# Performance work log

Measured on AMD Instinct MI355X. Metric: run time of the kernel, lower is better.

Reference implementation:

```python
import jax, jax.numpy as jnp
import numpy as np

V, E, H, B, S = 32000, 512, 1024, 128, 512
NEG = -1e9


def setup_inputs() -> dict:
    key = jax.random.key(0)
    ks = jax.random.split(key, 12)
    s = 0.02
    return {
        "previous_word": jax.random.randint(ks[0], (B, 1), 0, V),
        "h_0": jax.random.normal(ks[1], (B, H), jnp.float32),
        "c_0": jax.random.normal(ks[2], (B, H), jnp.float32),
        "ctx": jax.random.normal(ks[3], (B, S, H), jnp.float32),
        "ctx_mask": jnp.zeros((B, S), dtype=bool),
        "emb": jax.random.normal(ks[4], (V, E), jnp.float32) * s,
        "W_ih": jax.random.normal(ks[5], (4 * H, E), jnp.float32) * s,
        "W_hh": jax.random.normal(ks[6], (4 * H, H), jnp.float32) * s,
        "b_ih": jnp.zeros((4 * H,), jnp.float32),
        "b_hh": jnp.zeros((4 * H,), jnp.float32),
        "W_in": jax.random.normal(ks[7], (H, H), jnp.float32) * s,
        "W_out": jax.random.normal(ks[8], (H, 2 * H), jnp.float32) * s,
        "W_dec": jax.random.normal(ks[9], (V, H), jnp.float32) * s,
        "b_dec": jnp.zeros((V,), jnp.float32),
    }


def reference(previous_word, h_0, c_0, ctx, ctx_mask, emb, W_ih, W_hh, b_ih, b_hh, W_in, W_out, W_dec, b_dec):
    # embedding lookup + squeeze; dropout is identity in eval mode
    x = emb[previous_word[:, 0]]                       # [B, E]
    # LSTMCell: gate order i, f, g, o (PyTorch convention)
    gates = x @ W_ih.T + b_ih + h_0 @ W_hh.T + b_hh    # [B, 4H]
    i, f, g, o = jnp.split(gates, 4, axis=1)
    i = jax.nn.sigmoid(i)
    f = jax.nn.sigmoid(f)
    g = jnp.tanh(g)
    o = jax.nn.sigmoid(o)
    c_1 = f * c_0 + i * g
    h_1 = o * jnp.tanh(c_1)
    # SoftDotAttention
    target = h_1 @ W_in.T                               # [B, H]
    attn = jnp.einsum('bsh,bh->bs', ctx, target)        # [B, S]
    attn = jnp.where(ctx_mask, NEG, attn)
    alpha = jax.nn.softmax(attn, axis=1)
    weighted = jnp.einsum('bs,bsh->bh', alpha, ctx)     # [B, H]
    h_tilde = jnp.tanh(jnp.concatenate([weighted, h_1], axis=1) @ W_out.T)
    logit = h_tilde @ W_dec.T + b_dec                   # [B, V]
    return (h_1, c_1, alpha, logit)
```

## Files before the change

### kernel.cpp

```cpp
#include <hip/hip_runtime.h>
#include <hip/hip_bf16.h>
#include <cstdint>

#define NEG_BIG (-1.0e9f)

typedef __attribute__((ext_vector_type(8))) short short8_t;
typedef __attribute__((ext_vector_type(4))) float f32x4;

typedef __attribute__((address_space(1))) const unsigned int gu32_t;
typedef __attribute__((address_space(3))) unsigned int lu32_t;

__device__ __forceinline__ short f2bf(float x) {
  union { float f; unsigned u; } v; v.f = x;
  unsigned r = v.u + 0x7fffu + ((v.u >> 16) & 1u);
  return (short)(r >> 16);
}
__device__ __forceinline__ float sigmoidf_(float x) { return 1.0f / (1.0f + __expf(-x)); }

__device__ __forceinline__ void lds_barrier() {
  asm volatile("s_waitcnt lgkmcnt(0)\n\ts_barrier" ::: "memory");
}
__device__ __forceinline__ void block_barrier() {
  asm volatile("" ::: "memory");
  __builtin_amdgcn_s_barrier();
  asm volatile("" ::: "memory");
}

__global__ void k_pack_a1(const int* __restrict__ prev, const float* __restrict__ emb,
                          const float* __restrict__ h0, short* __restrict__ A1) {
  int t = blockIdx.x * 256 + threadIdx.x;
  if (t >= 128 * 1536) return;
  int b = t / 1536, k = t - b * 1536;
  float v = (k < 512) ? emb[(size_t)prev[b] * 512 + k] : h0[b * 1024 + (k - 512)];
  A1[t] = f2bf(v);
}

template <int MB, int WN, int EPI>
__launch_bounds__(256, 2)
__global__ void k_gemm(const short* __restrict__ A, int lda,
                       const float* __restrict__ Wa, int ldwa, int Ka,
                       const float* __restrict__ Wb, int ldwb, int Ktot,
                       const float* __restrict__ bias0, const float* __restrict__ bias1,
                       float* __restrict__ outF, short* __restrict__ outB, int ldo,
                       int kstride, size_t pstride) {
  constexpr int BN = WN * 16;
  constexpr int MREP = (MB == 128) ? 2 * WN : 1;
  constexpr int AU = MB / 32;
  constexpr int WLOADS = (BN * 64) / 1024;
  __shared__ __align__(16) short lA[2][MB * 64];
  __shared__ __align__(16) short lW[2][BN * 64];
  const int kc = blockIdx.z;
  A += (size_t)kc * kstride;
  Wa += (size_t)kc * kstride;
  if (outF) outF += (size_t)kc * pstride;
  const int tid = threadIdx.x;
  const int wid = tid >> 6, l = tid & 63, l15 = l & 15, khalf = l >> 4;
  const int nblk = blockIdx.x;
  const int mrow0 = blockIdx.y * MB;
  const int m_wave = (WN == 1) ? wid * (MB / 4) : 0;
  const int nb_local = (WN == 4) ? wid * 16 : 0;

  const int arow = (MB == 128) ? (tid >> 1) : (tid >> 2);
  const int apart = (MB == 128) ? (tid & 1) : (tid & 3);
  const int abase = apart * (AU * 16);
  const int aswz = (arow & 7) << 4;
  const short* Arow = A + (size_t)(mrow0 + arow) * lda + apart * (AU * 8);

  int wn_[WLOADS], wkq_[WLOADS];
#pragma unroll
  for (int j = 0; j < WLOADS; ++j) {
    int idx = j * 1024 + tid * 4;
    wn_[j] = idx >> 6;
    wkq_[j] = idx & 63;
  }

  f32x4 acc[MREP];
#pragma unroll
  for (int r = 0; r < MREP; ++r) acc[r] = (f32x4){0.f, 0.f, 0.f, 0.f};

  short8_t aR[AU];
  float4 wR[WLOADS];

  auto stage_regs = [&](int k0) {
#pragma unroll
    for (int q = 0; q < AU; ++q) aR[q] = *(const short8_t*)(Arow + k0 + q * 8);
#pragma unroll
    for (int j = 0; j < WLOADS; ++j) {
      int kg = k0 + wkq_[j];
      const float* p = (kg < Ka) ? (Wa + (size_t)(nblk * BN + wn_[j]) * ldwa + kg)
                                 : (Wb + (size_t)(nblk * BN + wn_[j]) * ldwb + (kg - Ka));
      wR[j] = *(const float4*)p;
    }
  };
  auto write_lds = [&](int buf) {
    char* drow = (char*)lA[buf] + arow * 128;
#pragma unroll
    for (int q = 0; q < AU; ++q)
      *(short8_t*)(drow + ((abase + q * 16) ^ aswz)) = aR[q];
#pragma unroll
    for (int j = 0; j < WLOADS; ++j) {
      short4 h4;
      h4.x = f2bf(wR[j].x); h4.y = f2bf(wR[j].y); h4.z = f2bf(wR[j].z); h4.w = f2bf(wR[j].w);
      *(short4*)((char*)lW[buf] + wn_[j] * 128 + ((wkq_[j] * 2) ^ ((wn_[j] & 7) << 4))) = h4;
    }
  };
  auto compute = [&](int buf) {
#pragma unroll
    for (int ks = 0; ks < 2; ++ks) {
      const int ubyte = ks * 64 + khalf * 16;
      const int nrow = nb_local + l15;
      short8_t bfrag = *(const short8_t*)((char*)lW[buf] + nrow * 128 + (ubyte ^ ((nrow & 7) << 4)));
#pragma unroll
      for (int r = 0; r < MREP; ++r) {
        const int mrow = m_wave + r * 16 + l15;
        short8_t afrag = *(const short8_t*)((char*)lA[buf] + mrow * 128 + (ubyte ^ ((mrow & 7) << 4)));
        acc[r] = __builtin_amdgcn_mfma_f32_16x16x32_bf16(afrag, bfrag, acc[r], 0, 0, 0);
      }
    }
  };

  const int NT = Ktot >> 6;
  stage_regs(0);
  write_lds(0);
  for (int t = 0; t < NT; ++t) {
    const int cur = t & 1;
    if (t + 1 < NT) stage_regs((t + 1) << 6);
    lds_barrier();
    compute(cur);
    if (t + 1 < NT) write_lds(cur ^ 1);
  }

  const int n = nblk * BN + nb_local + l15;
  float bias = 0.f;
  if (bias0) bias = bias0[n];
  if (bias1) bias += bias1[n];
#pragma unroll
  for (int r = 0; r < MREP; ++r) {
    int mb = mrow0 + m_wave + r * 16 + khalf * 4;
#pragma unroll
    for (int e = 0; e < 4; ++e) {
      float v = acc[r][e] + bias;
      if (EPI == 1) {
        outB[(size_t)(mb + e) * ldo + n] = f2bf(tanhf(v));
      } else {
        outF[(size_t)(mb + e) * ldo + n] = v;
      }
    }
  }
}

__global__ void k_lstm(const float* __restrict__ gates, const float* __restrict__ c0,
                       float* __restrict__ h1_out, float* __restrict__ c1_out,
                       short* __restrict__ A3) {
  int t = blockIdx.x * 256 + threadIdx.x;
  int b = t >> 10, h = t & 1023;
  const float* g = gates + (size_t)b * 4096;
  float ig = sigmoidf_(g[h]);
  float fg = sigmoidf_(g[1024 + h]);
  float gg = tanhf(g[2048 + h]);
  float og = sigmoidf_(g[3072 + h]);
  float c1 = fg * c0[t] + ig * gg;
  float h1 = og * tanhf(c1);
  c1_out[t] = c1;
  h1_out[t] = h1;
  A3[(size_t)b * 2048 + 1024 + h] = f2bf(h1);
}

__launch_bounds__(256, 2)
__global__ void k_attn(const float* __restrict__ ctx, const float* __restrict__ tp,
                       const unsigned char* __restrict__ mask,
                       float* __restrict__ scores, float* __restrict__ part) {
  __shared__ __align__(16) float lds[2][8 * 1024];
  const int b = blockIdx.x >> 2, chunk = blockIdx.x & 3;
  const int tid = threadIdx.x;
  const int wid = tid >> 6, l = tid & 63;
  float4 t4[4], w4[4];
#pragma unroll
  for (int j = 0; j < 4; ++j) {
    float4 a = {0.f, 0.f, 0.f, 0.f};
#pragma unroll
    for (int p = 0; p < 4; ++p) {
      const float4 v = *(const float4*)(tp + (size_t)p * 131072 + (size_t)b * 1024 + j * 256 + l * 4);
      a.x += v.x; a.y += v.y; a.z += v.z; a.w += v.w;
    }
    t4[j] = a;
    w4[j].x = 0.f; w4[j].y = 0.f; w4[j].z = 0.f; w4[j].w = 0.f;
  }
  float m = -INFINITY, lsum = 0.f;
  const int s0 = chunk * 128;
  const float* cb = ctx + ((size_t)b * 512 + s0) * 1024;
  const unsigned char* mk = mask + (size_t)b * 512 + s0;

  auto stage = [&](int buf, int tt) {
    const char* src = (const char*)(cb + (size_t)tt * 8192);
    char* dst = (char*)&lds[buf][0];
#pragma unroll
    for (int i = 0; i < 8; ++i) {
      const int off = i * 4096 + tid * 16;
      __builtin_amdgcn_global_load_lds((gu32_t*)(src + off), (lu32_t*)(dst + off), 16, 0, 0);
    }
  };

  stage(0, 0);
  int buf = 0;
  for (int t = 0; t < 16; ++t) {
    if (t < 15) {
      stage(buf ^ 1, t + 1);
      asm volatile("s_waitcnt vmcnt(8)" ::: "memory");
    } else {
      asm volatile("s_waitcnt vmcnt(0)" ::: "memory");
    }
    block_barrier();
#pragma unroll
    for (int rr = 0; rr < 2; ++rr) {
      const int r = wid * 2 + rr;
      const float* row = &lds[buf][r * 1024];
      float4 c0 = *(const float4*)(row + l * 4);
      float4 c1 = *(const float4*)(row + 256 + l * 4);
      float4 c2 = *(const float4*)(row + 512 + l * 4);
      float4 c3 = *(const float4*)(row + 768 + l * 4);
      float p = c0.x * t4[0].x + c0.y * t4[0].y + c0.z * t4[0].z + c0.w * t4[0].w +
                c1.x * t4[1].x + c1.y * t4[1].y + c1.z * t4[1].z + c1.w * t4[1].w +
                c2.x * t4[2].x + c2.y * t4[2].y + c2.z * t4[2].z + c2.w * t4[2].w +
                c3.x * t4[3].x + c3.y * t4[3].y + c3.z * t4[3].z + c3.w * t4[3].w;
#pragma unroll
      for (int off = 32; off > 0; off >>= 1) p += __shfl_xor(p, off);
      const int sg = t * 8 + r;
      if (mk[sg]) p = NEG_BIG;
      if (l == 0) scores[(size_t)b * 512 + s0 + sg] = p;
      float mn = fmaxf(m, p);
      float scale = __expf(m - mn);
      float e = __expf(p - mn);
      lsum = lsum * scale + e;
      w4[0].x = w4[0].x * scale + e * c0.x; w4[0].y = w4[0].y * scale + e * c0.y;
      w4[0].z = w4[0].z * scale + e * c0.z; w4[0].w = w4[0].w * scale + e * c0.w;
      w4[1].x = w4[1].x * scale + e * c1.x; w4[1].y = w4[1].y * scale + e * c1.y;
      w4[1].z = w4[1].z * scale + e * c1.z; w4[1].w = w4[1].w * scale + e * c1.w;
      w4[2].x = w4[2].x * scale + e * c2.x; w4[2].y = w4[2].y * scale + e * c2.y;
      w4[2].z = w4[2].z * scale + e * c2.z; w4[2].w = w4[2].w * scale + e * c2.w;
      w4[3].x = w4[3].x * scale + e * c3.x; w4[3].y = w4[3].y * scale + e * c3.y;
      w4[3].z = w4[3].z * scale + e * c3.z; w4[3].w = w4[3].w * scale + e * c3.w;
      m = mn;
    }
    block_barrier();
    buf ^= 1;
  }
  float* pp = part + ((size_t)b * 16 + (chunk * 4 + wid)) * 1028;
#pragma unroll
  for (int j = 0; j < 4; ++j) *(float4*)(pp + j * 256 + l * 4) = w4[j];
  if (l == 0) { pp[1024] = m; pp[1025] = lsum; }
}

__launch_bounds__(256, 4)
__global__ void k_finish(const float* __restrict__ scores, const float* __restrict__ part,
                         float* __restrict__ alpha, short* __restrict__ A3) {
  __shared__ float sm[16], sl[16];
  int b = blockIdx.x, t = threadIdx.x;
  if (t < 16) {
    sm[t] = part[((size_t)b * 16 + t) * 1028 + 1024];
    sl[t] = part[((size_t)b * 16 + t) * 1028 + 1025];
  }
  __syncthreads();
  float M = -INFINITY;
#pragma unroll
  for (int i = 0; i < 16; ++i) M = fmaxf(M, sm[i]);
  float scl[16];
  float L = 0.f;
#pragma unroll
  for (int i = 0; i < 16; ++i) {
    scl[i] = __expf(sm[i] - M);
    L += sl[i] * scl[i];
  }
  float inv = 1.0f / L;
  float s0 = scores[(size_t)b * 512 + t];
  float s1 = scores[(size_t)b * 512 + 256 + t];
  alpha[(size_t)b * 512 + t] = __expf(s0 - M) * inv;
  alpha[(size_t)b * 512 + 256 + t] = __expf(s1 - M) * inv;
  float ax = 0.f, ay = 0.f, az = 0.f, aw = 0.f;
#pragma unroll
  for (int i = 0; i < 16; ++i) {
    const float4 w = *(const float4*)(part + ((size_t)b * 16 + i) * 1028 + t * 4);
    ax += scl[i] * w.x; ay += scl[i] * w.y; az += scl[i] * w.z; aw += scl[i] * w.w;
  }
  short4 o4;
  o4.x = f2bf(ax * inv); o4.y = f2bf(ay * inv); o4.z = f2bf(az * inv); o4.w = f2bf(aw * inv);
  *(short4*)(A3 + (size_t)b * 2048 + t * 4) = o4;
}

__global__ void k_htilde(const float* __restrict__ wp, short* __restrict__ ht) {
  int t = blockIdx.x * 256 + threadIdx.x;
  float s = 0.f;
#pragma unroll
  for (int p = 0; p < 8; ++p) s += wp[(size_t)p * 131072 + t];
  ht[t] = f2bf(tanhf(s));
}

extern "C" void kernel_launch(void* const* d_in, const int* in_sizes, int n_in,
                              void* d_out, int out_size, void* d_ws, size_t ws_size,
                              hipStream_t stream) {
  const int* prev = (const int*)d_in[0];
  const float* h0 = (const float*)d_in[1];
  const float* c0 = (const float*)d_in[2];
  const float* ctx = (const float*)d_in[3];
  const unsigned char* mask = (const unsigned char*)d_in[4];
  const float* emb = (const float*)d_in[5];
  const float* W_ih = (const float*)d_in[6];
  const float* W_hh = (const float*)d_in[7];
  const float* b_ih = (const float*)d_in[8];
  const float* b_hh = (const float*)d_in[9];
  const float* W_in = (const float*)d_in[10];
  const float* W_out = (const float*)d_in[11];
  const float* W_dec = (const float*)d_in[12];
  const float* b_dec = (const float*)d_in[13];

  float* out_h1 = (float*)d_out;
  float* out_c1 = out_h1 + 128 * 1024;
  float* out_alpha = out_c1 + 128 * 1024;
  float* out_logit = out_alpha + 128 * 512;

  char* ws = (char*)d_ws;
  short* A3 = (short*)(ws + 0x000000);
  float* scores = (float*)(ws + 0x100000);
  float* tp = (float*)(ws + 0x200000);
  float* part = (float*)(ws + 0x400000);
  float* wp = (float*)(ws + 0xD00000);
  float* gates = (float*)(ws + 0x1100000);
  short* A1 = (short*)(ws + 0x1300000);
  short* htilde = (short*)(ws + 0x1400000);

  k_pack_a1<<<768, 256, 0, stream>>>(prev, emb, h0, A1);
  k_gemm<128, 1, 0><<<dim3(256, 1, 1), 256, 0, stream>>>(
      A1, 1536, W_ih, 512, 512, W_hh, 1024, 1536, b_ih, b_hh, gates, nullptr, 4096, 0, 0);
  k_lstm<<<512, 256, 0, stream>>>(gates, c0, out_h1, out_c1, A3);
  k_gemm<128, 1, 0><<<dim3(64, 1, 4), 256, 0, stream>>>(
      A3 + 1024, 2048, W_in, 1024, 1 << 30, W_in, 1024, 256, nullptr, nullptr, tp, nullptr,
      1024, 256, (size_t)131072);
  k_attn<<<512, 256, 0, stream>>>(ctx, tp, mask, scores, part);
  k_finish<<<128, 256, 0, stream>>>(scores, part, out_alpha, A3);
  k_gemm<128, 1, 0><<<dim3(64, 1, 8), 256, 0, stream>>>(
      A3, 2048, W_out, 2048, 1 << 30, W_out, 2048, 256, nullptr, nullptr, wp, nullptr,
      1024, 256, (size_t)131072);
  k_htilde<<<512, 256, 0, stream>>>(wp, htilde);
  k_gemm<128, 4, 0><<<dim3(500, 1, 1), 256, 0, stream>>>(
      htilde, 1024, W_dec, 1024, 1024, W_dec, 1024, 1024, b_dec, nullptr, out_logit, nullptr,
      32000, 0, 0);
}
```

Baseline: 134.3 us.

## Fuse embedding gather into gate GEMM and pre-reduce attention partials per block

Replaces the separate pack kernel plus generic gate GEMM with a dedicated kernel that gathers embedding rows and h_0 directly from global memory, converts them to bf16 in registers and stages them in LDS, removing one launch and the A1 round trip. Inside the attention kernel the four per-wave online-softmax partials are merged through LDS before being written, so the finish kernel reads 4 partials per batch instead of 16. This cuts partial-buffer traffic, at the cost of an extra block-wide barrier and LDS pass at the end of attention. The fused GEMM also redoes the bf16 conversion of the A tile in every one of its 256 blocks.

```diff
diff --git a/kernel.cpp b/kernel.cpp
--- a/kernel.cpp
+++ b/kernel.cpp
@@ -26,13 +26,89 @@
   asm volatile("" ::: "memory");
 }
 
-__global__ void k_pack_a1(const int* __restrict__ prev, const float* __restrict__ emb,
-                          const float* __restrict__ h0, short* __restrict__ A1) {
-  int t = blockIdx.x * 256 + threadIdx.x;
-  if (t >= 128 * 1536) return;
-  int b = t / 1536, k = t - b * 1536;
-  float v = (k < 512) ? emb[(size_t)prev[b] * 512 + k] : h0[b * 1024 + (k - 512)];
-  A1[t] = f2bf(v);
+__launch_bounds__(256, 2)
+__global__ void k_ggemm(const int* __restrict__ prev, const float* __restrict__ emb,
+                        const float* __restrict__ h0,
+                        const float* __restrict__ W_ih, const float* __restrict__ W_hh,
+                        const float* __restrict__ b_ih, const float* __restrict__ b_hh,
+                        float* __restrict__ gates) {
+  __shared__ __align__(16) short lA[2][128 * 64];
+  __shared__ __align__(16) short lW[2][16 * 64];
+  const int tid = threadIdx.x;
+  const int wid = tid >> 6, l = tid & 63, l15 = l & 15, khalf = l >> 4;
+  const int nblk = blockIdx.x;
+
+  const int arow = tid >> 1, apart = tid & 1;
+  const int aswz = (arow & 7) << 4;
+  const float* embrow = emb + (size_t)prev[arow] * 512;
+  const float* h0row = h0 + (size_t)arow * 1024;
+
+  const int wn = (tid * 4) >> 6;
+  const int wkq = (tid * 4) & 63;
+  const float* wih = W_ih + (size_t)(nblk * 16 + wn) * 512;
+  const float* whh = W_hh + (size_t)(nblk * 16 + wn) * 1024;
+
+  f32x4 acc[2];
+  acc[0] = (f32x4){0.f, 0.f, 0.f, 0.f};
+  acc[1] = (f32x4){0.f, 0.f, 0.f, 0.f};
+
+  float4 aF[8], wR;
+  auto stage_regs = [&](int k0) {
+    const int col0 = k0 + apart * 32;
+    const float* asrc = (col0 < 512) ? (embrow + col0) : (h0row + (col0 - 512));
+#pragma unroll
+    for (int q = 0; q < 8; ++q) aF[q] = *(const float4*)(asrc + q * 4);
+    const int kg = k0 + wkq;
+    wR = (kg < 512) ? *(const float4*)(wih + kg) : *(const float4*)(whh + (kg - 512));
+  };
+  auto write_lds = [&](int buf) {
+    char* drow = (char*)lA[buf] + arow * 128;
+#pragma unroll
+    for (int q = 0; q < 4; ++q) {
+      short8_t s;
+      s[0] = f2bf(aF[2 * q].x); s[1] = f2bf(aF[2 * q].y);
+      s[2] = f2bf(aF[2 * q].z); s[3] = f2bf(aF[2 * q].w);
+      s[4] = f2bf(aF[2 * q + 1].x); s[5] = f2bf(aF[2 * q + 1].y);
+      s[6] = f2bf(aF[2 * q + 1].z); s[7] = f2bf(aF[2 * q + 1].w);
+      *(short8_t*)(drow + ((apart * 64 + q * 16) ^ aswz)) = s;
+    }
+    short4 h4;
+    h4.x = f2bf(wR.x); h4.y = f2bf(wR.y); h4.z = f2bf(wR.z); h4.w = f2bf(wR.w);
+    *(short4*)((char*)lW[buf] + wn * 128 + ((wkq * 2) ^ ((wn & 7) << 4))) = h4;
+  };
+  auto compute = [&](int buf) {
+#pragma unroll
+    for (int ks = 0; ks < 2; ++ks) {
+      const int ubyte = ks * 64 + khalf * 16;
+      short8_t bfrag = *(const short8_t*)((char*)lW[buf] + l15 * 128 + (ubyte ^ ((l15 & 7) << 4)));
+#pragma unroll
+      for (int r = 0; r < 2; ++r) {
+        const int mrow = wid * 32 + r * 16 + l15;
+        short8_t afrag = *(const short8_t*)((char*)lA[buf] + mrow * 128 + (ubyte ^ ((mrow & 7) << 4)));
+        acc[r] = __builtin_amdgcn_mfma_f32_16x16x32_bf16(afrag, bfrag, acc[r], 0, 0, 0);
+      }
+    }
+  };
+
+  stage_regs(0);
+  write_lds(0);
+  for (int t = 0; t < 24; ++t) {
+    const int cur = t & 1;
+    if (t + 1 < 24) stage_regs((t + 1) << 6);
+    lds_barrier();
+    compute(cur);
+    if (t + 1 < 24) write_lds(cur ^ 1);
+  }
+
+  const int n = nblk * 16 + l15;
+  const float bias = b_ih[n] + b_hh[n];
+#pragma unroll
+  for (int r = 0; r < 2; ++r) {
+    int mb = wid * 32 + r * 16 + khalf * 4;
+#pragma unroll
+    for (int e = 0; e < 4; ++e)
+      gates[(size_t)(mb + e) * 4096 + n] = acc[r][e] + bias;
+  }
 }
 
 template <int MB, int WN, int EPI>
@@ -171,6 +247,7 @@
                        const unsigned char* __restrict__ mask,
                        float* __restrict__ scores, float* __restrict__ part) {
   __shared__ __align__(16) float lds[2][8 * 1024];
+  __shared__ float sml[8];
   const int b = blockIdx.x >> 2, chunk = blockIdx.x & 3;
   const int tid = threadIdx.x;
   const int wid = tid >> 6, l = tid & 63;
@@ -245,29 +322,45 @@
     block_barrier();
     buf ^= 1;
   }
-  float* pp = part + ((size_t)b * 16 + (chunk * 4 + wid)) * 1028;
-#pragma unroll
-  for (int j = 0; j < 4; ++j) *(float4*)(pp + j * 256 + l * 4) = w4[j];
-  if (l == 0) { pp[1024] = m; pp[1025] = lsum; }
+
+  float* cbuf = &lds[0][0];
+#pragma unroll
+  for (int j = 0; j < 4; ++j) *(float4*)(cbuf + wid * 1024 + j * 256 + l * 4) = w4[j];
+  if (l == 0) { sml[wid] = m; sml[4 + wid] = lsum; }
+  __syncthreads();
+  const float M = fmaxf(fmaxf(sml[0], sml[1]), fmaxf(sml[2], sml[3]));
+  const float sc0 = __expf(sml[0] - M), sc1 = __expf(sml[1] - M);
+  const float sc2 = __expf(sml[2] - M), sc3 = __expf(sml[3] - M);
+  const float L = sml[4] * sc0 + sml[5] * sc1 + sml[6] * sc2 + sml[7] * sc3;
+  const float4 v0 = *(const float4*)(cbuf + 0 * 1024 + tid * 4);
+  const float4 v1 = *(const float4*)(cbuf + 1 * 1024 + tid * 4);
+  const float4 v2 = *(const float4*)(cbuf + 2 * 1024 + tid * 4);
+  const float4 v3 = *(const float4*)(cbuf + 3 * 1024 + tid * 4);
+  float4 o;
+  o.x = v0.x * sc0 + v1.x * sc1 + v2.x * sc2 + v3.x * sc3;
+  o.y = v0.y * sc0 + v1.y * sc1 + v2.y * sc2 + v3.y * sc3;
+  o.z = v0.z * sc0 + v1.z * sc1 + v2.z * sc2 + v3.z * sc3;
+  o.w = v0.w * sc0 + v1.w * sc1 + v2.w * sc2 + v3.w * sc3;
+  float* pp = part + ((size_t)b * 4 + chunk) * 1028;
+  *(float4*)(pp + tid * 4) = o;
+  if (tid == 0) { pp[1024] = M; pp[1025] = L; }
 }
 
 __launch_bounds__(256, 4)
 __global__ void k_finish(const float* __restrict__ scores, const float* __restrict__ part,
                          float* __restrict__ alpha, short* __restrict__ A3) {
-  __shared__ float sm[16], sl[16];
+  __shared__ float sm[4], sl[4];
   int b = blockIdx.x, t = threadIdx.x;
-  if (t < 16) {
-    sm[t] = part[((size_t)b * 16 + t) * 1028 + 1024];
-    sl[t] = part[((size_t)b * 16 + t) * 1028 + 1025];
+  if (t < 4) {
+    sm[t] = part[((size_t)b * 4 + t) * 1028 + 1024];
+    sl[t] = part[((size_t)b * 4 + t) * 1028 + 1025];
   }
   __syncthreads();
-  float M = -INFINITY;
-#pragma unroll
-  for (int i = 0; i < 16; ++i) M = fmaxf(M, sm[i]);
-  float scl[16];
+  float M = fmaxf(fmaxf(sm[0], sm[1]), fmaxf(sm[2], sm[3]));
+  float scl[4];
   float L = 0.f;
 #pragma unroll
-  for (int i = 0; i < 16; ++i) {
+  for (int i = 0; i < 4; ++i) {
     scl[i] = __expf(sm[i] - M);
     L += sl[i] * scl[i];
   }
@@ -278,8 +371,8 @@
   alpha[(size_t)b * 512 + 256 + t] = __expf(s1 - M) * inv;
   float ax = 0.f, ay = 0.f, az = 0.f, aw = 0.f;
 #pragma unroll
-  for (int i = 0; i < 16; ++i) {
-    const float4 w = *(const float4*)(part + ((size_t)b * 16 + i) * 1028 + t * 4);
+  for (int i = 0; i < 4; ++i) {
+    const float4 w = *(const float4*)(part + ((size_t)b * 4 + i) * 1028 + t * 4);
     ax += scl[i] * w.x; ay += scl[i] * w.y; az += scl[i] * w.z; aw += scl[i] * w.w;
   }
   short4 o4;
@@ -325,12 +418,9 @@
   float* part = (float*)(ws + 0x400000);
   float* wp = (float*)(ws + 0xD00000);
   float* gates = (float*)(ws + 0x1100000);
-  short* A1 = (short*)(ws + 0x1300000);
   short* htilde = (short*)(ws + 0x1400000);
 
-  k_pack_a1<<<768, 256, 0, stream>>>(prev, emb, h0, A1);
-  k_gemm<128, 1, 0><<<dim3(256, 1, 1), 256, 0, stream>>>(
-      A1, 1536, W_ih, 512, 512, W_hh, 1024, 1536, b_ih, b_hh, gates, nullptr, 4096, 0, 0);
+  k_ggemm<<<256, 256, 0, stream>>>(prev, emb, h0, W_ih, W_hh, b_ih, b_hh, gates);
   k_lstm<<<512, 256, 0, stream>>>(gates, c0, out_h1, out_c1, A3);
   k_gemm<128, 1, 0><<<dim3(64, 1, 4), 256, 0, stream>>>(
       A3 + 1024, 2048, W_in, 1024, 1 << 30, W_in, 1024, 256, nullptr, nullptr, tp, nullptr,
```

Result: slower. 143.5 us (+6.9%).
